# Performance work log

Hardware: AMD Instinct MI355X
Metric: run time of the kernel (lower is better)

The kernel has to match this reference:

```python
import jax, jax.numpy as jnp
import numpy as np

D, H, DH, DF = 128, 8, 16, 512
N_Q, N_KV, E = 20000, 20000, 640000


def _xavier(key, shape):
    fan_in, fan_out = shape[1], shape[0]
    lim = float(np.sqrt(6.0 / (fan_in + fan_out)))
    return jax.random.uniform(key, shape, jnp.float32, -lim, lim)


def layer_norm(x, g, b, eps=1e-5):
    mu = jnp.mean(x, axis=-1, keepdims=True)
    var = jnp.var(x, axis=-1, keepdims=True)
    return (x - mu) * jax.lax.rsqrt(var + eps) * g + b


def setup_inputs() -> dict:
    key = jax.random.key(0)
    ks = jax.random.split(key, 12)
    return {
        "q_feat": jax.random.normal(ks[0], (N_Q, D), jnp.float32),
        "kv_feat": jax.random.normal(ks[1], (N_KV, D), jnp.float32),
        "src": jax.random.randint(ks[2], (E,), 0, N_KV, jnp.int32),
        "dst": jax.random.randint(ks[3], (E,), 0, N_Q, jnp.int32),
        "Wq": _xavier(ks[4], (H * DH, D)),
        "Wk": _xavier(ks[5], (H * DH, D)),
        "Wv": _xavier(ks[6], (H * DH, D)),
        "Wo": _xavier(ks[7], (D, H * DH)),
        "W1": _xavier(ks[8], (DF, D)),
        "bf1": jnp.zeros((DF,), jnp.float32),
        "W2": _xavier(ks[9], (D, DF)),
        "bf2": jnp.zeros((D,), jnp.float32),
        "ln1_g": jnp.ones((D,), jnp.float32),
        "ln1_b": jnp.zeros((D,), jnp.float32),
        "ln2_g": jnp.ones((D,), jnp.float32),
        "ln2_b": jnp.zeros((D,), jnp.float32),
    }


def reference(q_feat, kv_feat, src, dst, Wq, Wk, Wv, Wo, W1, bf1, W2, bf2,
              ln1_g, ln1_b, ln2_g, ln2_b):
    n_q = q_feat.shape[0]
    # projections -> [N, H, DH]
    q = (q_feat @ Wq.T).reshape(-1, H, DH)
    k = (kv_feat @ Wk.T).reshape(-1, H, DH)
    v = (kv_feat @ Wv.T).reshape(-1, H, DH)
    # edge scores: u_mul_v then sum over d_head, scaled (score per edge per head)
    score = jnp.einsum('ehd,ehd->eh', k[src], q[dst]) / np.sqrt(DH)
    # edge_softmax grouped by destination node
    mx = jax.ops.segment_max(score, dst, num_segments=n_q)  # [Nq, H]
    ex = jnp.exp(score - mx[dst])
    denom = jax.ops.segment_sum(ex, dst, num_segments=n_q)
    att = ex / denom[dst]  # [E, H]
    # weighted scatter-sum of values to destination nodes
    msg = v[src] * att[:, :, None]  # [E, H, DH]
    out = jax.ops.segment_sum(msg, dst, num_segments=n_q)  # [Nq, H, DH]
    sa = out.reshape(n_q, H * DH) @ Wo.T
    feat = layer_norm(q_feat + sa, ln1_g, ln1_b)
    ff = jax.nn.relu(feat @ W1.T + bf1) @ W2.T + bf2
    return layer_norm(feat + ff, ln2_g, ln2_b)
```

## Files before the change

kernel.cpp:

```cpp
#include <hip/hip_runtime.h>
#include <hip/hip_fp16.h>
#include <math.h>
#include <type_traits>

#define D 128
#define NH 8
#define DHD 16
#define DF 512
#define STR 128

typedef _Float16 half8 __attribute__((ext_vector_type(8)));
typedef _Float16 half4 __attribute__((ext_vector_type(4)));
typedef float f32x4 __attribute__((ext_vector_type(4)));


__global__ __launch_bounds__(256) void mega_kernel(
    const float* __restrict__ q_feat, const float* __restrict__ kv_feat,
    const float* __restrict__ Wq, const float* __restrict__ Wk,
    const float* __restrict__ Wv,
    __half* __restrict__ fq, __half* __restrict__ fkv, int NQ, int NKV,
    const int* __restrict__ dst, const int* __restrict__ src,
    int* __restrict__ cnt, int* __restrict__ srcg, int E,
    const float* __restrict__ Wo, const float* __restrict__ W1,
    const float* __restrict__ W2,
    __half* __restrict__ wo16, __half* __restrict__ w116, __half* __restrict__ w216) {
    __shared__ __align__(16) __half As[128 * 128];
    __shared__ __align__(16) __half Ws[64 * 128];

    int xt = blockIdx.x;
    int tid = threadIdx.x;

    if (xt >= 2) {
        if (xt == 18) {
            int g = blockIdx.y * 256 + tid;
            if (g < 36864) {
                const float* s;
                __half* d;
                int idx = g;
                if (idx < 4096) { s = Wo; d = wo16; }
                else if (idx < 20480) { idx -= 4096; s = W1; d = w116; }
                else { idx -= 20480; s = W2; d = w216; }
                float4 f = ((const float4*)s)[idx];
                ushort4 o;
                o.x = __half_as_ushort(__float2half(f.x));
                o.y = __half_as_ushort(__float2half(f.y));
                o.z = __half_as_ushort(__float2half(f.z));
                o.w = __half_as_ushort(__float2half(f.w));
                ((ushort4*)d)[idx] = o;
            }
            return;
        }
        int b = (xt - 2) * gridDim.y + blockIdx.y;
        int i = b * 256 + tid;
        if (i < E) {
            int dn = dst[i];
            int p = atomicAdd(&cnt[dn], 1);
            if (p < STR) srcg[((size_t)dn << 7) + p] = src[i];
        }
        return;
    }

    const float* A = xt ? kv_feat : q_feat;
    __half* C = xt ? fkv : fq;
    int O = xt ? 256 : 128;
    int NCT = xt ? 4 : 2;
    int N = xt ? NKV : NQ;
    int row0 = blockIdx.y * 128;
    if (row0 >= N) return;

    int lane = tid & 63;
    int w = tid >> 6;
    int wm = w >> 1, wn = w & 1;
    int l16 = lane & 15, lq = lane >> 4;

#pragma unroll
    for (int i = 0; i < 8; ++i) {
        int f = tid + i * 256;
        int ln = f & 63;
        int mt = (f >> 6) & 7;
        int kc = f >> 9;
        int m = row0 + mt * 16 + (ln & 15);
        int k = kc * 32 + (ln >> 4) * 8;
        half8 v = {};
        if (m < N) {
            const float4* p = (const float4*)(A + (size_t)m * 128 + k);
            float4 f0 = p[0], f1 = p[1];
            v = (half8){(_Float16)f0.x, (_Float16)f0.y, (_Float16)f0.z, (_Float16)f0.w,
                        (_Float16)f1.x, (_Float16)f1.y, (_Float16)f1.z, (_Float16)f1.w};
        }
        ((half8*)As)[f] = v;
    }

    for (int ct = 0; ct < NCT; ++ct) {
        __syncthreads();
#pragma unroll
        for (int i = 0; i < 4; ++i) {
            int f = tid + i * 256;
            int ln = f & 63;
            int nt = (f >> 6) & 3;
            int kc = f >> 8;
            int n = ct * 64 + nt * 16 + (ln & 15);
            int k = kc * 32 + (ln >> 4) * 8;
            const float* Wsrc;
            int r;
            if (xt == 0) {
                Wsrc = Wq; r = n;
            } else {
                int h = n >> 5, qd = (n >> 3) & 3, isv = (n >> 2) & 1, d2 = n & 3;
                r = h * 16 + qd * 4 + d2;
                Wsrc = isv ? Wv : Wk;
            }
            const float4* p = (const float4*)(Wsrc + (size_t)r * 128 + k);
            float4 f0 = p[0], f1 = p[1];
            ((half8*)Ws)[f] = (half8){(_Float16)f0.x, (_Float16)f0.y, (_Float16)f0.z, (_Float16)f0.w,
                                      (_Float16)f1.x, (_Float16)f1.y, (_Float16)f1.z, (_Float16)f1.w};
        }
        __syncthreads();
        f32x4 acc[4][2];
#pragma unroll
        for (int i = 0; i < 4; ++i)
#pragma unroll
            for (int j = 0; j < 2; ++j) acc[i][j] = (f32x4){0.f, 0.f, 0.f, 0.f};
#pragma unroll
        for (int kc = 0; kc < 4; ++kc) {
            half8 a[4], b[2];
#pragma unroll
            for (int i = 0; i < 4; ++i) a[i] = ((half8*)As)[(kc * 8 + wm * 4 + i) * 64 + lane];
#pragma unroll
            for (int j = 0; j < 2; ++j) b[j] = ((half8*)Ws)[(kc * 4 + wn * 2 + j) * 64 + lane];
#pragma unroll
            for (int i = 0; i < 4; ++i)
#pragma unroll
                for (int j = 0; j < 2; ++j)
                    acc[i][j] = __builtin_amdgcn_mfma_f32_16x16x32_f16(a[i], b[j], acc[i][j], 0, 0, 0);
        }
#pragma unroll
        for (int i = 0; i < 4; ++i) {
            int rbase = row0 + (wm * 4 + i) * 16 + lq * 4;
#pragma unroll
            for (int j = 0; j < 2; ++j) {
                int c = ct * 64 + (wn * 2 + j) * 16 + l16;
#pragma unroll
                for (int r = 0; r < 4; ++r) {
                    int row = rbase + r;
                    if (row < N) C[(size_t)row * O + c] = __float2half(acc[i][j][r]);
                }
            }
        }
    }
}


__global__ __launch_bounds__(256) void attn_kernel(
    const __half* __restrict__ q, const __half* __restrict__ kv,
    const int* __restrict__ srcg, const int* __restrict__ cnt,
    __half* __restrict__ out, int NQ) {
    int n = blockIdx.x * 4 + (threadIdx.x >> 6);
    if (n >= NQ) return;
    int lane = threadIdx.x & 63;
    int eh = lane >> 5;
    int sub = lane & 31;
    int doff = sub << 2;
    half4 q4 = *(const half4*)(q + (size_t)n * D + doff);
    float q0 = (float)q4[0] * 0.25f, q1 = (float)q4[1] * 0.25f;
    float q2 = (float)q4[2] * 0.25f, q3 = (float)q4[3] * 0.25f;
    int s0 = n << 7;
    int c_ = cnt[n];
    int s1 = s0 + (c_ < STR ? c_ : STR);
    float lA = 0.f, lB = 0.f, lC = 0.f, lD = 0.f;
    f32x4 aA = {0.f, 0.f, 0.f, 0.f}, aB = {0.f, 0.f, 0.f, 0.f};
    f32x4 aC = {0.f, 0.f, 0.f, 0.f}, aD = {0.f, 0.f, 0.f, 0.f};
    int j = s0;
    for (; j + 8 <= s1; j += 8) {
        int e0 = srcg[j + eh];
        int e1 = srcg[j + 2 + eh];
        int e2 = srcg[j + 4 + eh];
        int e3 = srcg[j + 6 + eh];
        half8 c0 = *(const half8*)(kv + (size_t)e0 * 256 + (sub << 3));
        half8 c1 = *(const half8*)(kv + (size_t)e1 * 256 + (sub << 3));
        half8 c2 = *(const half8*)(kv + (size_t)e2 * 256 + (sub << 3));
        half8 c3 = *(const half8*)(kv + (size_t)e3 * 256 + (sub << 3));
        float p0 = q0 * (float)c0[0] + q1 * (float)c0[1] + q2 * (float)c0[2] + q3 * (float)c0[3];
        float p1 = q0 * (float)c1[0] + q1 * (float)c1[1] + q2 * (float)c1[2] + q3 * (float)c1[3];
        float p2 = q0 * (float)c2[0] + q1 * (float)c2[1] + q2 * (float)c2[2] + q3 * (float)c2[3];
        float p3 = q0 * (float)c3[0] + q1 * (float)c3[1] + q2 * (float)c3[2] + q3 * (float)c3[3];
        p0 += __shfl_xor(p0, 1, 4); p0 += __shfl_xor(p0, 2, 4);
        p1 += __shfl_xor(p1, 1, 4); p1 += __shfl_xor(p1, 2, 4);
        p2 += __shfl_xor(p2, 1, 4); p2 += __shfl_xor(p2, 2, 4);
        p3 += __shfl_xor(p3, 1, 4); p3 += __shfl_xor(p3, 2, 4);
        float x0 = __expf(fminf(p0, 70.f));
        float x1 = __expf(fminf(p1, 70.f));
        float x2 = __expf(fminf(p2, 70.f));
        float x3 = __expf(fminf(p3, 70.f));
        lA += x0; lB += x1; lC += x2; lD += x3;
        aA[0] += x0 * (float)c0[4]; aA[1] += x0 * (float)c0[5];
        aA[2] += x0 * (float)c0[6]; aA[3] += x0 * (float)c0[7];
        aB[0] += x1 * (float)c1[4]; aB[1] += x1 * (float)c1[5];
        aB[2] += x1 * (float)c1[6]; aB[3] += x1 * (float)c1[7];
        aC[0] += x2 * (float)c2[4]; aC[1] += x2 * (float)c2[5];
        aC[2] += x2 * (float)c2[6]; aC[3] += x2 * (float)c2[7];
        aD[0] += x3 * (float)c3[4]; aD[1] += x3 * (float)c3[5];
        aD[2] += x3 * (float)c3[6]; aD[3] += x3 * (float)c3[7];
    }
    for (; j + 4 <= s1; j += 4) {
        int e0 = srcg[j + eh];
        int e1 = srcg[j + 2 + eh];
        half8 c0 = *(const half8*)(kv + (size_t)e0 * 256 + (sub << 3));
        half8 c1 = *(const half8*)(kv + (size_t)e1 * 256 + (sub << 3));
        float p0 = q0 * (float)c0[0] + q1 * (float)c0[1] + q2 * (float)c0[2] + q3 * (float)c0[3];
        float p1 = q0 * (float)c1[0] + q1 * (float)c1[1] + q2 * (float)c1[2] + q3 * (float)c1[3];
        p0 += __shfl_xor(p0, 1, 4); p0 += __shfl_xor(p0, 2, 4);
        p1 += __shfl_xor(p1, 1, 4); p1 += __shfl_xor(p1, 2, 4);
        float x0 = __expf(fminf(p0, 70.f));
        float x1 = __expf(fminf(p1, 70.f));
        lA += x0; lB += x1;
        aA[0] += x0 * (float)c0[4]; aA[1] += x0 * (float)c0[5];
        aA[2] += x0 * (float)c0[6]; aA[3] += x0 * (float)c0[7];
        aB[0] += x1 * (float)c1[4]; aB[1] += x1 * (float)c1[5];
        aB[2] += x1 * (float)c1[6]; aB[3] += x1 * (float)c1[7];
    }
    for (; j < s1; j += 2) {
        bool valid = (j + eh) < s1;
        int e0 = srcg[valid ? (j + eh) : s0];
        half8 c0 = *(const half8*)(kv + (size_t)e0 * 256 + (sub << 3));
        float p0 = q0 * (float)c0[0] + q1 * (float)c0[1] + q2 * (float)c0[2] + q3 * (float)c0[3];
        p0 += __shfl_xor(p0, 1, 4); p0 += __shfl_xor(p0, 2, 4);
        float x0 = valid ? __expf(fminf(p0, 70.f)) : 0.f;
        lA += x0;
        aA[0] += x0 * (float)c0[4]; aA[1] += x0 * (float)c0[5];
        aA[2] += x0 * (float)c0[6]; aA[3] += x0 * (float)c0[7];
    }
    float l = (lA + lB) + (lC + lD);
    f32x4 a;
#pragma unroll
    for (int i = 0; i < 4; ++i) a[i] = (aA[i] + aB[i]) + (aC[i] + aD[i]);
    l += __shfl_xor(l, 32);
#pragma unroll
    for (int i = 0; i < 4; ++i) a[i] += __shfl_xor(a[i], 32);
    if (eh == 0) {
        float rl = (l > 0.f) ? 1.f / l : 0.f;
        half4 o = {(_Float16)(a[0] * rl), (_Float16)(a[1] * rl),
                   (_Float16)(a[2] * rl), (_Float16)(a[3] * rl)};
        *(half4*)(out + (size_t)n * D + doff) = o;
    }
}


__device__ __forceinline__ int feat_idx64(int rr, int mt, int c) {
    return (((c >> 5) * 4 + mt) * 64 + ((c >> 3) & 3) * 16 + rr) * 8 + (c & 7);
}

__global__ __launch_bounds__(256) void tail_kernel(
    const __half* __restrict__ A , const __half* __restrict__ Wo16,
    const float* __restrict__ res1 ,
    const float* __restrict__ g1, const float* __restrict__ b1,
    const __half* __restrict__ W1h, const float* __restrict__ fb1,
    const __half* __restrict__ W2h, const float* __restrict__ fb2,
    const float* __restrict__ g2, const float* __restrict__ b2,
    float* __restrict__ out, int N) {
    __shared__ __align__(16) __half Feat[64 * 128];
    __shared__ __align__(16) __half S1[64 * 128];
    __shared__ __align__(16) __half S2[128 * 64];
    __shared__ __align__(16) __half Hs[64 * 64];
    int tid = threadIdx.x, lane = tid & 63, w = tid >> 6;
    int row0 = blockIdx.x * 64;
    int l16 = lane & 15, lq = lane >> 4;

#pragma unroll
    for (int i = 0; i < 4; ++i) {
        int f = tid + i * 256;
        int ln = f & 63, mt = (f >> 6) & 3, kc = f >> 8;
        int m = row0 + mt * 16 + (ln & 15);
        int k = kc * 32 + (ln >> 4) * 8;
        half8 av = {};
        if (m < N) av = *(const half8*)(A + (size_t)m * D + k);
        ((half8*)S1)[f] = av;
    }

    f32x4 acc[8];
#pragma unroll
    for (int j = 0; j < 8; ++j) acc[j] = (f32x4){0.f, 0.f, 0.f, 0.f};
#pragma unroll
    for (int kt = 0; kt < 2; ++kt) {
        __syncthreads();
#pragma unroll
        for (int i = 0; i < 4; ++i) {
            int f = tid + i * 256;
            int ln = f & 63, ot = (f >> 6) & 7, kc2 = f >> 9;
            int o = ot * 16 + (ln & 15);
            int k = kt * 64 + kc2 * 32 + (ln >> 4) * 8;
            ((half8*)S2)[f] = *(const half8*)(Wo16 + (size_t)o * D + k);
        }
        __syncthreads();
#pragma unroll
        for (int kc2 = 0; kc2 < 2; ++kc2) {
            half8 a = ((half8*)S1)[((kt * 2 + kc2) * 4 + w) * 64 + lane];
            half8 bf[8];
#pragma unroll
            for (int j = 0; j < 8; ++j) bf[j] = ((half8*)S2)[(kc2 * 8 + j) * 64 + lane];
#pragma unroll
            for (int j = 0; j < 8; ++j)
                acc[j] = __builtin_amdgcn_mfma_f32_16x16x32_f16(a, bf[j], acc[j], 0, 0, 0);
        }
    }
    __syncthreads();

#pragma unroll
    for (int r = 0; r < 4; ++r) {
        int rr = lq * 4 + r;
        int row = row0 + w * 16 + rr;
        bool valid = row < N;
        float vals[8];
        float s = 0.f, sq = 0.f;
#pragma unroll
        for (int j = 0; j < 8; ++j) {
            int c = j * 16 + l16;
            float v = acc[j][r];
            if (valid) v += res1[(size_t)row * D + c];
            vals[j] = v;
            s += v;
            sq += v * v;
        }
#pragma unroll
        for (int m = 1; m < 16; m <<= 1) {
            s += __shfl_xor(s, m, 16);
            sq += __shfl_xor(sq, m, 16);
        }
        float mu = s * (1.f / 128.f);
        float var = sq * (1.f / 128.f) - mu * mu;
        float inv = rsqrtf(var + 1e-5f);
#pragma unroll
        for (int j = 0; j < 8; ++j) {
            int c = j * 16 + l16;
            float o = (vals[j] - mu) * inv * g1[c] + b1[c];
            Feat[feat_idx64(rr, w, c)] = __float2half(o);
        }
    }
    __syncthreads();

    half8 a_all[4];
#pragma unroll
    for (int kc = 0; kc < 4; ++kc)
        a_all[kc] = ((half8*)Feat)[(kc * 4 + w) * 64 + lane];

    f32x4 oacc[8];
#pragma unroll
    for (int j = 0; j < 8; ++j) oacc[j] = (f32x4){0.f, 0.f, 0.f, 0.f};

    for (int hc = 0; hc < 8; ++hc) {
        __syncthreads();
#pragma unroll
        for (int i = 0; i < 4; ++i) {
            int f = tid + i * 256;
            int ln = f & 63, nt = (f >> 6) & 3, kc = f >> 8;
            int n = hc * 64 + nt * 16 + (ln & 15);
            int k = kc * 32 + (ln >> 4) * 8;
            ((half8*)S1)[f] = *(const half8*)(W1h + (size_t)n * D + k);
        }
#pragma unroll
        for (int i = 0; i < 4; ++i) {
            int f = tid + i * 256;
            int ln = f & 63, ot = (f >> 6) & 7, kc2 = f >> 9;
            int o = ot * 16 + (ln & 15);
            int k = hc * 64 + kc2 * 32 + (ln >> 4) * 8;
            ((half8*)S2)[f] = *(const half8*)(W2h + (size_t)o * DF + k);
        }
        __syncthreads();
        f32x4 hacc[4];
#pragma unroll
        for (int j = 0; j < 4; ++j) hacc[j] = (f32x4){0.f, 0.f, 0.f, 0.f};
#pragma unroll
        for (int kc = 0; kc < 4; ++kc) {
            half8 b[4];
#pragma unroll
            for (int j = 0; j < 4; ++j) b[j] = ((half8*)S1)[(kc * 4 + j) * 64 + lane];
#pragma unroll
            for (int j = 0; j < 4; ++j)
                hacc[j] = __builtin_amdgcn_mfma_f32_16x16x32_f16(a_all[kc], b[j], hacc[j], 0, 0, 0);
        }
#pragma unroll
        for (int j = 0; j < 4; ++j) {
            float bias1 = fb1[hc * 64 + j * 16 + l16];
#pragma unroll
            for (int r = 0; r < 4; ++r) {
                float v = fmaxf(hacc[j][r] + bias1, 0.f);
                int kc2 = j >> 1;
                int lanep = ((j & 1) * 2 + (l16 >> 3)) * 16 + lq * 4 + r;
                Hs[((kc2 * 4 + w) * 64 + lanep) * 8 + (l16 & 7)] = __float2half(v);
            }
        }
        __syncthreads();
#pragma unroll
        for (int kc2 = 0; kc2 < 2; ++kc2) {
            half8 a = ((half8*)Hs)[(kc2 * 4 + w) * 64 + lane];
            half8 b[8];
#pragma unroll
            for (int ot = 0; ot < 8; ++ot) b[ot] = ((half8*)S2)[(kc2 * 8 + ot) * 64 + lane];
#pragma unroll
            for (int ot = 0; ot < 8; ++ot)
                oacc[ot] = __builtin_amdgcn_mfma_f32_16x16x32_f16(a, b[ot], oacc[ot], 0, 0, 0);
        }
    }

#pragma unroll
    for (int r = 0; r < 4; ++r) {
        int rr = lq * 4 + r;
        int row = row0 + w * 16 + rr;
        bool valid = row < N;
        float vals[8];
        float s = 0.f, sq = 0.f;
#pragma unroll
        for (int j = 0; j < 8; ++j) {
            int c = j * 16 + l16;
            float v = oacc[j][r] + fb2[c] + __half2float(Feat[feat_idx64(rr, w, c)]);
            vals[j] = v;
            s += v;
            sq += v * v;
        }
#pragma unroll
        for (int m = 1; m < 16; m <<= 1) {
            s += __shfl_xor(s, m, 16);
            sq += __shfl_xor(sq, m, 16);
        }
        float mu = s * (1.f / 128.f);
        float var = sq * (1.f / 128.f) - mu * mu;
        float inv = rsqrtf(var + 1e-5f);
        if (valid) {
#pragma unroll
            for (int j = 0; j < 8; ++j) {
                int c = j * 16 + l16;
                out[(size_t)row * D + c] = (vals[j] - mu) * inv * g2[c] + b2[c];
            }
        }
    }
}


extern "C" void kernel_launch(void* const* d_in, const int* in_sizes, int n_in,
                              void* d_out, int out_size, void* d_ws, size_t ws_size,
                              hipStream_t stream) {
    const float* q_feat = (const float*)d_in[0];
    const float* kv_feat = (const float*)d_in[1];
    const int* src = (const int*)d_in[2];
    const int* dst = (const int*)d_in[3];
    const float* Wq = (const float*)d_in[4];
    const float* Wk = (const float*)d_in[5];
    const float* Wv = (const float*)d_in[6];
    const float* Wo = (const float*)d_in[7];
    const float* W1 = (const float*)d_in[8];
    const float* bf1 = (const float*)d_in[9];
    const float* W2 = (const float*)d_in[10];
    const float* bf2 = (const float*)d_in[11];
    const float* ln1g = (const float*)d_in[12];
    const float* ln1b = (const float*)d_in[13];
    const float* ln2g = (const float*)d_in[14];
    const float* ln2b = (const float*)d_in[15];

    int NQ = in_sizes[0] / D;
    int NKV = in_sizes[1] / D;
    int E = in_sizes[2];
    float* out = (float*)d_out;

    char* base = (char*)d_ws;
    size_t off = 0;
    auto alloc = [&](size_t bytes) -> void* {
        void* p = base + off;
        off += (bytes + 255) & ~(size_t)255;
        return p;
    };
    __half* fq16 = (__half*)alloc((size_t)NQ * D * 2);
    __half* fkv = (__half*)alloc((size_t)NKV * 256 * 2);
    __half* fattn16 = (__half*)alloc((size_t)NQ * D * 2);
    int* cnt = (int*)alloc((size_t)NQ * 4);
    int* srcg = (int*)alloc((size_t)NQ * STR * 4);
    __half* wo16 = (__half*)alloc((size_t)D * D * 2);
    __half* w116 = (__half*)alloc((size_t)DF * D * 2);
    __half* w216 = (__half*)alloc((size_t)D * DF * 2);

    hipMemsetAsync(cnt, 0, (size_t)NQ * sizeof(int), stream);

    dim3 blk(256);
    int NMX = NQ > NKV ? NQ : NKV;
    int ytiles = (NMX + 127) / 128;
    mega_kernel<<<dim3(19, ytiles), blk, 0, stream>>>(
        q_feat, kv_feat, Wq, Wk, Wv, fq16, fkv, NQ, NKV,
        dst, src, cnt, srcg, E, Wo, W1, W2, wo16, w116, w216);

    attn_kernel<<<(NQ + 3) / 4, blk, 0, stream>>>(fq16, fkv, srcg, cnt, fattn16, NQ);

    tail_kernel<<<(NQ + 63) / 64, blk, 0, stream>>>(
        fattn16, wo16, q_feat, ln1g, ln1b, w116, bf1, w216, bf2, ln2g, ln2b, out, NQ);
}
```

Measured before the change: 214.9 us.

## Bucket edges by destination range in LDS counters, drop global memset

Edge bucketing no longer uses one thread per edge with global atomics. Now 64 blocks each scan the whole dst array with int4 loads and keep only the edges whose destination falls in their range, counting them with LDS atomics. The counts are then written to global memory directly, so the separate memset launch goes away. Each block reads all 640K dst values, so total read traffic grows about 64x, and only 64 blocks do the bucketing, which may make this branch the critical path in the fused kernel.

```diff
diff --git a/kernel.cpp b/kernel.cpp
--- a/kernel.cpp
+++ b/kernel.cpp
@@ -8,6 +8,7 @@
 #define DHD 16
 #define DF 512
 #define STR 128
+#define NFB 64
 
 typedef _Float16 half8 __attribute__((ext_vector_type(8)));
 typedef _Float16 half4 __attribute__((ext_vector_type(4)));
@@ -30,33 +31,71 @@
     int xt = blockIdx.x;
     int tid = threadIdx.x;
 
-    if (xt >= 2) {
-        if (xt == 18) {
-            int g = blockIdx.y * 256 + tid;
-            if (g < 36864) {
-                const float* s;
-                __half* d;
-                int idx = g;
-                if (idx < 4096) { s = Wo; d = wo16; }
-                else if (idx < 20480) { idx -= 4096; s = W1; d = w116; }
-                else { idx -= 20480; s = W2; d = w216; }
-                float4 f = ((const float4*)s)[idx];
-                ushort4 o;
-                o.x = __half_as_ushort(__float2half(f.x));
-                o.y = __half_as_ushort(__float2half(f.y));
-                o.z = __half_as_ushort(__float2half(f.z));
-                o.w = __half_as_ushort(__float2half(f.w));
-                ((ushort4*)d)[idx] = o;
-            }
-            return;
-        }
-        int b = (xt - 2) * gridDim.y + blockIdx.y;
-        int i = b * 256 + tid;
-        if (i < E) {
+    if (xt == 3) {
+        int g = blockIdx.y * 256 + tid;
+        if (g < 36864) {
+            const float* s;
+            __half* d;
+            int idx = g;
+            if (idx < 4096) { s = Wo; d = wo16; }
+            else if (idx < 20480) { idx -= 4096; s = W1; d = w116; }
+            else { idx -= 20480; s = W2; d = w216; }
+            float4 f = ((const float4*)s)[idx];
+            ushort4 o;
+            o.x = __half_as_ushort(__float2half(f.x));
+            o.y = __half_as_ushort(__float2half(f.y));
+            o.z = __half_as_ushort(__float2half(f.z));
+            o.w = __half_as_ushort(__float2half(f.w));
+            ((ushort4*)d)[idx] = o;
+        }
+        return;
+    }
+
+    if (xt == 2) {
+        int fb = blockIdx.y;
+        if (fb >= NFB) return;
+        int chunk = (NQ + NFB - 1) / NFB;
+        int dlo = fb * chunk;
+        int dhi = dlo + chunk < NQ ? dlo + chunk : NQ;
+        if (dlo >= NQ) return;
+        int* lcnt = (int*)As;
+        for (int i = tid; i < chunk; i += 256) lcnt[i] = 0;
+        __syncthreads();
+        int E4 = E >> 2;
+        for (int i4 = tid; i4 < E4; i4 += 256) {
+            int4 d4 = ((const int4*)dst)[i4];
+            int ii = i4 << 2;
+            int dn;
+            dn = d4.x;
+            if (dn >= dlo && dn < dhi) {
+                int p = atomicAdd(&lcnt[dn - dlo], 1);
+                if (p < STR) srcg[((size_t)dn << 7) + p] = src[ii];
+            }
+            dn = d4.y;
+            if (dn >= dlo && dn < dhi) {
+                int p = atomicAdd(&lcnt[dn - dlo], 1);
+                if (p < STR) srcg[((size_t)dn << 7) + p] = src[ii + 1];
+            }
+            dn = d4.z;
+            if (dn >= dlo && dn < dhi) {
+                int p = atomicAdd(&lcnt[dn - dlo], 1);
+                if (p < STR) srcg[((size_t)dn << 7) + p] = src[ii + 2];
+            }
+            dn = d4.w;
+            if (dn >= dlo && dn < dhi) {
+                int p = atomicAdd(&lcnt[dn - dlo], 1);
+                if (p < STR) srcg[((size_t)dn << 7) + p] = src[ii + 3];
+            }
+        }
+        for (int i = (E4 << 2) + tid; i < E; i += 256) {
             int dn = dst[i];
-            int p = atomicAdd(&cnt[dn], 1);
-            if (p < STR) srcg[((size_t)dn << 7) + p] = src[i];
-        }
+            if (dn >= dlo && dn < dhi) {
+                int p = atomicAdd(&lcnt[dn - dlo], 1);
+                if (p < STR) srcg[((size_t)dn << 7) + p] = src[i];
+            }
+        }
+        __syncthreads();
+        for (int i = tid; i < dhi - dlo; i += 256) cnt[dlo + i] = lcnt[i];
         return;
     }
 
@@ -477,12 +516,10 @@
     __half* w116 = (__half*)alloc((size_t)DF * D * 2);
     __half* w216 = (__half*)alloc((size_t)D * DF * 2);
 
-    hipMemsetAsync(cnt, 0, (size_t)NQ * sizeof(int), stream);
-
     dim3 blk(256);
     int NMX = NQ > NKV ? NQ : NKV;
     int ytiles = (NMX + 127) / 128;
-    mega_kernel<<<dim3(19, ytiles), blk, 0, stream>>>(
+    mega_kernel<<<dim3(4, ytiles), blk, 0, stream>>>(
         q_feat, kv_feat, Wq, Wk, Wv, fq16, fkv, NQ, NKV,
         dst, src, cnt, srcg, E, Wo, W1, W2, wo16, w116, w216);
 
```

Result: slower. 583.5 us (+171.5%).
